# Kernel tuning notes

Hardware: AMD Instinct MI355X
Metric: run time of the kernel (lower is better)

The kernel has to match this reference:

```python
import jax, jax.numpy as jnp
import numpy as np

B, F, V, E = 65536, 39, 100000, 16
EPS = 1e-5

def setup_inputs() -> dict:
    key = jax.random.key(0)
    ks = jax.random.split(key, 10)
    return {
        'Xi': jax.random.randint(ks[0], (B, F, 1), 0, V, dtype=jnp.int64) if jax.config.read('jax_enable_x64') else jax.random.randint(ks[0], (B, F, 1), 0, V, dtype=jnp.int32),
        'Xv': jax.random.uniform(ks[1], (B, F), dtype=jnp.float32),
        'emb1': jax.random.normal(ks[2], (F, V, 1), dtype=jnp.float32),
        'emb2': jax.random.normal(ks[3], (F, V, E), dtype=jnp.float32),
        'W1': jax.random.normal(ks[4], (F * E, 512), dtype=jnp.float32) * 0.02,
        'b1': jax.random.normal(ks[5], (512,), dtype=jnp.float32) * 0.02,
        'g1': jnp.ones((512,), jnp.float32),
        'be1': jnp.zeros((512,), jnp.float32),
        'W2': jax.random.normal(ks[6], (512, 256), dtype=jnp.float32) * 0.02,
        'b2': jax.random.normal(ks[7], (256,), dtype=jnp.float32) * 0.02,
        'g2': jnp.ones((256,), jnp.float32),
        'be2': jnp.zeros((256,), jnp.float32),
        'bias': jax.random.normal(ks[8], (1,), dtype=jnp.float32),
    }

def _batchnorm(x, g, b):
    mu = jnp.mean(x, axis=0)
    var = jnp.mean(jnp.square(x - mu), axis=0)  # biased var, torch BN training mode
    return (x - mu) * jax.lax.rsqrt(var + EPS) * g + b

def reference(Xi, Xv, emb1, emb2, W1, b1, g1, be1, W2, b2, g2, be2, bias):
    idx = Xi[:, :, 0]                                # [B, F]
    fidx = jnp.arange(F)[None, :]                    # [1, F]
    # fused per-field gathers: [B, F] and [B, F, E]
    first = emb1[fidx, idx, 0] * Xv                  # first-order, [B, F]
    fm2 = emb2[fidx, idx] * Xv[:, :, None]           # second-order embeds, [B, F, E]
    sum_emb = jnp.sum(fm2, axis=1)                   # [B, E]
    second = 0.5 * (jnp.square(sum_emb) - jnp.sum(jnp.square(fm2), axis=1))  # [B, E]
    # deep part (note: original forward never applies the final num_classes layer)
    deep = fm2.reshape(B, F * E)
    deep = _batchnorm(deep @ W1 + b1, g1, be1)
    deep = _batchnorm(deep @ W2 + b2, g2, be2)
    return bias + jnp.sum(first, axis=1) + jnp.sum(second, axis=1) + jnp.sum(deep, axis=1)
```

## Files before the change

kernel.cpp:

```cpp
#include <hip/hip_runtime.h>

#define B_ROWS 65536
#define F_FEAT 39
#define V_VOC  100000
#define D_PAD  640
#define BN_EPS 1e-5f

typedef __bf16 bf16x8 __attribute__((ext_vector_type(8)));
typedef float  f32x16 __attribute__((ext_vector_type(16)));

__device__ __forceinline__ unsigned short toBF(float x) {
  unsigned int u = __float_as_uint(x);
  u += 0x7fffu + ((u >> 16) & 1u);
  return (unsigned short)(u >> 16);
}
__device__ __forceinline__ unsigned int pk2(float a, float b) {
  return (unsigned int)toBF(a) | ((unsigned int)toBF(b) << 16);
}

__global__ __launch_bounds__(256) void k0_prep(
    const int* __restrict__ Xi, const float* __restrict__ Xv,
    int* __restrict__ XiT, float* __restrict__ XvT,
    float* __restrict__ M, unsigned short* __restrict__ XT) {
  for (int i = threadIdx.x; i < 800; i += 256)
    M[(size_t)blockIdx.x * 800 + i] = 0.f;

  const int b0 = blockIdx.x * 128;
  for (int u = threadIdx.x; u < 16 * 128; u += 256) {
    int m = 624 + (u >> 7), j = u & 127;
    XT[(size_t)m * B_ROWS + b0 + j] = (m == 624) ? (unsigned short)0x3f80 : (unsigned short)0;
  }

  __shared__ int   ti[128][41];
  __shared__ float tv[128][41];
  for (int u = threadIdx.x; u < 128 * 39; u += 256) {
    int r = u / 39, f = u - r * 39;
    ti[r][f] = Xi[(size_t)b0 * 39 + u];
    tv[r][f] = Xv[(size_t)b0 * 39 + u];
  }
  __syncthreads();
  for (int u = threadIdx.x; u < 39 * 128; u += 256) {
    int f = u >> 7, j = u & 127;
    XiT[(size_t)f * B_ROWS + b0 + j] = ti[j][f];
    XvT[(size_t)f * B_ROWS + b0 + j] = tv[j][f];
  }
}

__global__ __launch_bounds__(1024) void k1g_gather(
    const int* __restrict__ XiT, const float* __restrict__ XvT,
    const float* __restrict__ emb1, const float* __restrict__ emb2,
    unsigned short* __restrict__ XB, float* __restrict__ FS1) {
  const int tid = blockIdx.x * 1024 + threadIdx.x;
  for (int e = tid; e < F_FEAT * B_ROWS; e += 256 * 1024) {
    const int f = e >> 16;
    const int id = XiT[e];
    const float xv = XvT[e];
    const float4* er = reinterpret_cast<const float4*>(emb2 + ((size_t)f * V_VOC + id) * 16);
    float4 q0 = er[0], q1 = er[1], q2 = er[2], q3 = er[3];
    float e1 = emb1[(size_t)f * V_VOC + id];
    uint4 d0, d1;
    d0.x = pk2(q0.x * xv, q0.y * xv); d0.y = pk2(q0.z * xv, q0.w * xv);
    d0.z = pk2(q1.x * xv, q1.y * xv); d0.w = pk2(q1.z * xv, q1.w * xv);
    d1.x = pk2(q2.x * xv, q2.y * xv); d1.y = pk2(q2.z * xv, q2.w * xv);
    d1.z = pk2(q3.x * xv, q3.y * xv); d1.w = pk2(q3.z * xv, q3.w * xv);
    uint4* dst = reinterpret_cast<uint4*>(XB + (size_t)e * 16);
    dst[0] = d0; dst[1] = d1;
    FS1[e] = e1 * xv;
  }
}

__global__ __launch_bounds__(256) void k_transpose(const unsigned short* __restrict__ XB,
                                                   unsigned short* __restrict__ XT) {
  const int f = blockIdx.y;
  const int b0 = blockIdx.x * 512;
  __shared__ unsigned int ls[16][257];
  const int t = threadIdx.x;
  const int bb = b0 + 2 * t;
  const uint4* s0 = reinterpret_cast<const uint4*>(XB + ((size_t)f * B_ROWS + bb) * 16);
  uint4 qa0 = s0[0], qa1 = s0[1], qb0 = s0[2], qb1 = s0[3];
  const unsigned short* pa0 = reinterpret_cast<const unsigned short*>(&qa0);
  const unsigned short* pa1 = reinterpret_cast<const unsigned short*>(&qa1);
  const unsigned short* pb0 = reinterpret_cast<const unsigned short*>(&qb0);
  const unsigned short* pb1 = reinterpret_cast<const unsigned short*>(&qb1);
#pragma unroll
  for (int d = 0; d < 8; ++d) {
    ls[d][t]     = (unsigned)pa0[d] | ((unsigned)pb0[d] << 16);
    ls[d + 8][t] = (unsigned)pa1[d] | ((unsigned)pb1[d] << 16);
  }
  __syncthreads();
#pragma unroll
  for (int d = 0; d < 16; ++d) {
    unsigned int* row = reinterpret_cast<unsigned int*>(
        XT + (size_t)(f * 16 + d) * B_ROWS + b0);
    row[t] = ls[d][t];
  }
}

#define KSPLIT 32
__global__ __launch_bounds__(256) void k2_syrk(const unsigned short* __restrict__ XT,
                                               float* __restrict__ M) {
  const int p = blockIdx.x;
  const int xcd = p & 7;
  const int ks = ((p >> 3) / 15) * 8 + xcd;
  int pair = (p >> 3) % 15;
  int ti = 0;
  while (pair >= 5 - ti) { pair -= 5 - ti; ++ti; }
  const int tj = ti + pair;

  __shared__ unsigned short pa[128 * 64];
  __shared__ unsigned short pb[128 * 64];

  const int lane = threadIdx.x & 63, wid = threadIdx.x >> 6;
  const int wm = wid >> 1, wn = wid & 1;
  const int rl = lane & 31, hh = lane >> 5;

  f32x16 acc00, acc01, acc10, acc11;
#pragma unroll
  for (int i = 0; i < 16; ++i) { acc00[i] = 0.f; acc01[i] = 0.f; acc10[i] = 0.f; acc11[i] = 0.f; }

  const int krange = B_ROWS / KSPLIT;
  const int kbase = ks * krange;

  for (int kt = 0; kt < krange; kt += 64) {
    const int k0 = kbase + kt;
#pragma unroll
    for (int g2 = 0; g2 < 4; ++g2) {
      const int g = threadIdx.x + g2 * 256;
      const int r = g >> 3, j = g & 7;
      uint4 va = *reinterpret_cast<const uint4*>(XT + (size_t)(ti * 128 + r) * B_ROWS + k0 + j * 8);
      *reinterpret_cast<uint4*>((char*)pa + r * 128 + ((j ^ (r & 7)) << 4)) = va;
      uint4 vb = *reinterpret_cast<const uint4*>(XT + (size_t)(tj * 128 + r) * B_ROWS + k0 + j * 8);
      *reinterpret_cast<uint4*>((char*)pb + r * 128 + ((j ^ (r & 7)) << 4)) = vb;
    }
    __syncthreads();
#pragma unroll
    for (int kc = 0; kc < 4; ++kc) {
      const int ra0 = wm * 64 + rl, ra1 = wm * 64 + 32 + rl;
      const int rb0 = wn * 64 + rl, rb1 = wn * 64 + 32 + rl;
      bf16x8 a0 = *reinterpret_cast<const bf16x8*>((char*)pa + ra0 * 128 + (((kc * 2 + hh) ^ (ra0 & 7)) << 4));
      bf16x8 a1 = *reinterpret_cast<const bf16x8*>((char*)pa + ra1 * 128 + (((kc * 2 + hh) ^ (ra1 & 7)) << 4));
      bf16x8 b0 = *reinterpret_cast<const bf16x8*>((char*)pb + rb0 * 128 + (((kc * 2 + hh) ^ (rb0 & 7)) << 4));
      bf16x8 b1 = *reinterpret_cast<const bf16x8*>((char*)pb + rb1 * 128 + (((kc * 2 + hh) ^ (rb1 & 7)) << 4));
      acc00 = __builtin_amdgcn_mfma_f32_32x32x16_bf16(a0, b0, acc00, 0, 0, 0);
      acc01 = __builtin_amdgcn_mfma_f32_32x32x16_bf16(a0, b1, acc01, 0, 0, 0);
      acc10 = __builtin_amdgcn_mfma_f32_32x32x16_bf16(a1, b0, acc10, 0, 0, 0);
      acc11 = __builtin_amdgcn_mfma_f32_32x32x16_bf16(a1, b1, acc11, 0, 0, 0);
    }
    __syncthreads();
  }

#pragma unroll
  for (int rr = 0; rr < 16; ++rr) {
    const int rloc = (rr & 3) + ((rr >> 2) << 3) + hh * 4;
    const int row0 = ti * 128 + wm * 64 + rloc;
    const int row1 = row0 + 32;
    const int col0 = tj * 128 + wn * 64 + rl;
    atomicAdd(&M[row0 * D_PAD + col0], acc00[rr]);
    atomicAdd(&M[row0 * D_PAD + col0 + 32], acc01[rr]);
    atomicAdd(&M[row1 * D_PAD + col0], acc10[rr]);
    atomicAdd(&M[row1 * D_PAD + col0 + 32], acc11[rr]);
  }
}

__device__ __forceinline__ float fetchM(const float* M, int a, int b) {
  if ((a >> 7) > (b >> 7)) { int t = a; a = b; b = t; }
  return M[a * D_PAD + b];
}
__global__ void k3a_cov(const float* __restrict__ M, float* __restrict__ Cov,
                        float* __restrict__ mu) {
  const int i = blockIdx.x;
  const float inv = 1.f / 65536.f;
  const float mui = fetchM(M, 624, i) * inv;
  for (int j = threadIdx.x; j < D_PAD; j += 256) {
    float muj = fetchM(M, 624, j) * inv;
    Cov[i * D_PAD + j] = fetchM(M, i, j) * inv - mui * muj;
    if (i == 0) mu[j] = muj;
  }
}

__global__ __launch_bounds__(256) void qform(const float* __restrict__ Cov,
                                             const float* __restrict__ W, const int ldw,
                                             const float* __restrict__ g,
                                             float* __restrict__ alpha) {
  const int k0 = blockIdx.x * 2;
  __shared__ float w0s[624], w1s[624];
  for (int i = threadIdx.x; i < 624; i += 256) {
    w0s[i] = W[(size_t)i * ldw + k0];
    w1s[i] = W[(size_t)i * ldw + k0 + 1];
  }
  __syncthreads();
  const int j0 = threadIdx.x, j1 = threadIdx.x + 256, j2 = threadIdx.x + 512;
  const bool v2 = (j2 < 624);
  const float wj00 = w0s[j0], wj01 = w0s[j1], wj02 = v2 ? w0s[j2] : 0.f;
  const float wj10 = w1s[j0], wj11 = w1s[j1], wj12 = v2 ? w1s[j2] : 0.f;
  float acc0 = 0.f, acc1 = 0.f;
  for (int i = 0; i < 624; ++i) {
    const float wi0 = w0s[i], wi1 = w1s[i];
    const float* row = Cov + i * D_PAD;
    const float c0 = row[j0], c1 = row[j1], c2 = v2 ? row[j2] : 0.f;
    acc0 += wi0 * (c0 * wj00 + c1 * wj01 + c2 * wj02);
    acc1 += wi1 * (c0 * wj10 + c1 * wj11 + c2 * wj12);
  }
#pragma unroll
  for (int off = 32; off > 0; off >>= 1) {
    acc0 += __shfl_down(acc0, off);
    acc1 += __shfl_down(acc1, off);
  }
  __shared__ float pr[2][4];
  const int lane = threadIdx.x & 63, wv = threadIdx.x >> 6;
  if (lane == 0) { pr[0][wv] = acc0; pr[1][wv] = acc1; }
  __syncthreads();
  if (threadIdx.x == 0) {
    float v0 = pr[0][0] + pr[0][1] + pr[0][2] + pr[0][3];
    float v1 = pr[1][0] + pr[1][1] + pr[1][2] + pr[1][3];
    alpha[k0]     = g[k0]     * rsqrtf(v0 + BN_EPS);
    alpha[k0 + 1] = g[k0 + 1] * rsqrtf(v1 + BN_EPS);
  }
}

__global__ __launch_bounds__(256) void k3c_G(const float* __restrict__ W1,
                                             const float* __restrict__ alpha1,
                                             const float* __restrict__ W2,
                                             float* __restrict__ G) {
  const int i = blockIdx.x;
  __shared__ float a[512];
  for (int k = threadIdx.x; k < 512; k += 256)
    a[k] = W1[(size_t)i * 512 + k] * alpha1[k];
  __syncthreads();
  const int j = threadIdx.x;
  float acc = 0.f;
#pragma unroll 8
  for (int k = 0; k < 512; ++k) acc += a[k] * W2[(size_t)k * 256 + j];
  G[(size_t)i * 256 + j] = acc;
}

__global__ __launch_bounds__(256) void k3e_final(const float* __restrict__ G,
                                                 const float* __restrict__ alpha2,
                                                 const float* __restrict__ mu,
                                                 const float* __restrict__ be2,
                                                 const float* __restrict__ bias,
                                                 float* __restrict__ gw,
                                                 float* __restrict__ consts) {
  __shared__ float a2[256];
  __shared__ float gws[640];
  a2[threadIdx.x] = alpha2[threadIdx.x];
  __syncthreads();
  for (int i = threadIdx.x; i < 640; i += 256) {
    float acc = 0.f;
    if (i < 624) {
      const float* gr = G + (size_t)i * 256;
#pragma unroll 8
      for (int j = 0; j < 256; ++j) acc += gr[j] * a2[j];
    }
    gw[i] = acc;
    gws[i] = acc;
  }
  __syncthreads();
  float pm = 0.f;
  for (int i = threadIdx.x; i < 624; i += 256) pm += mu[i] * gws[i];
  float val = be2[threadIdx.x] - pm;
#pragma unroll
  for (int off = 32; off > 0; off >>= 1) val += __shfl_down(val, off);
  __shared__ float pr[4];
  const int lane = threadIdx.x & 63, wv = threadIdx.x >> 6;
  if (lane == 0) pr[wv] = val;
  __syncthreads();
  if (threadIdx.x == 0) consts[0] = bias[0] + pr[0] + pr[1] + pr[2] + pr[3];
}

__global__ __launch_bounds__(256) void k5_out(const float* __restrict__ FS1,
                                              const unsigned short* __restrict__ XT,
                                              const float* __restrict__ gw,
                                              const float* __restrict__ consts,
                                              float* __restrict__ out) {
  __shared__ float g[624];
  for (int m = threadIdx.x; m < 624; m += 256) g[m] = gw[m];
  __syncthreads();
  const int r = threadIdx.x >> 1, h = threadIdx.x & 1;
  const int b = blockIdx.x * 128 + r;
  const unsigned short* col = XT + b;

  float lin = 0.f, ssq = 0.f;
  float ps[16];
#pragma unroll
  for (int e = 0; e < 16; ++e) ps[e] = 0.f;

  const int m0 = h ? 320 : 0, m1 = h ? 624 : 320;
  for (int mo = m0; mo < m1; mo += 16) {
#pragma unroll
    for (int e = 0; e < 16; ++e) {
      const int m = mo + e;
      float x = __uint_as_float((unsigned int)col[(size_t)m * B_ROWS] << 16);
      lin += g[m] * x;
      ssq += x * x;
      ps[e] += x;
    }
  }
  const int fb = h ? 20 : 0, fe = h ? 39 : 20;
  for (int f = fb; f < fe; ++f)
    lin += FS1[(size_t)f * B_ROWS + b];

  float s2 = 0.f;
#pragma unroll
  for (int e = 0; e < 16; ++e) {
    float t = ps[e] + __shfl_xor(ps[e], 1);
    s2 += t * t;
  }
  float tot = lin + 0.5f * (0.5f * s2 - ssq);
  tot += __shfl_xor(tot, 1);
  if (h == 0) out[b] = tot + consts[0];
}

extern "C" void kernel_launch(void* const* d_in, const int* in_sizes, int n_in,
                              void* d_out, int out_size, void* d_ws, size_t ws_size,
                              hipStream_t stream) {
  const int*   Xi   = (const int*)d_in[0];
  const float* Xv   = (const float*)d_in[1];
  const float* emb1 = (const float*)d_in[2];
  const float* emb2 = (const float*)d_in[3];
  const float* W1   = (const float*)d_in[4];
  const float* g1   = (const float*)d_in[6];
  const float* W2   = (const float*)d_in[8];
  const float* g2   = (const float*)d_in[10];
  const float* be2  = (const float*)d_in[11];
  const float* bias = (const float*)d_in[12];
  float* out = (float*)d_out;
  char* ws = (char*)d_ws;

  const size_t SZ_XT  = (size_t)D_PAD * B_ROWS * 2;
  const size_t SZ_XB  = (size_t)F_FEAT * B_ROWS * 32;
  const size_t SZ_FB  = (size_t)F_FEAT * B_ROWS * 4;

  size_t off = 0;
  unsigned short* XT = (unsigned short*)(ws + off); off += SZ_XT;
  unsigned short* XB = (unsigned short*)(ws + off); off += SZ_XB;
  float* M    = (float*)(ws + off); off += (size_t)D_PAD * D_PAD * 4;
  float* COV  = (float*)(ws + off); off += (size_t)D_PAD * D_PAD * 4;
  float* MU   = (float*)(ws + off); off += D_PAD * 4;
  float* A1   = (float*)(ws + off); off += 512 * 4;
  float* A2   = (float*)(ws + off); off += 256 * 4;
  float* G    = (float*)(ws + off); off += (size_t)624 * 256 * 4;
  float* GW   = (float*)(ws + off); off += D_PAD * 4;
  float* CN   = (float*)(ws + off); off += 256;
  int*   XIT  = (int*)(ws + off);   off += SZ_FB;
  float* XVT  = (float*)(ws + off); off += SZ_FB;
  float* FS1  = (float*)(ws + off); off += SZ_FB;

  k0_prep<<<512, 256, 0, stream>>>(Xi, Xv, XIT, XVT, M, XT);
  k1g_gather<<<256, 1024, 0, stream>>>(XIT, XVT, emb1, emb2, XB, FS1);
  k_transpose<<<dim3(128, F_FEAT), 256, 0, stream>>>(XB, XT);
  k2_syrk<<<15 * KSPLIT, 256, 0, stream>>>(XT, M);
  k3a_cov<<<D_PAD, 256, 0, stream>>>(M, COV, MU);
  qform<<<256, 256, 0, stream>>>(COV, W1, 512, g1, A1);
  k3c_G<<<624, 256, 0, stream>>>(W1, A1, W2, G);
  qform<<<128, 256, 0, stream>>>(COV, G, 256, g2, A2);
  k3e_final<<<1, 256, 0, stream>>>(G, A2, MU, be2, bias, GW, CN);
  k5_out<<<512, 256, 0, stream>>>(FS1, XT, GW, CN, out);
}
```

Measured before the change: 412.7 us.

## Partition embedding gather by XCD with table-half prefetch into L2

The gather is restructured so that each group of blocks sharing an XCD (blockIdx mod 8) handles a fixed set of 78 table slices (field, half-vocab). For each slice the 32 blocks first stream the whole ~3.2MB half-table into the local L2 with coalesced loads, then gather only the rows whose index falls in that half. Output stores are made nontemporal. The aim is to turn random HBM gathers into L2-resident hits. In exchange every index is read twice, the full tables are streamed regardless of use, and the scheme relies on round-robin block-to-XCD placement, with no sync ensuring the prefetch lands before the gathers.

```diff
diff --git a/kernel.cpp b/kernel.cpp
--- a/kernel.cpp
+++ b/kernel.cpp
@@ -3,11 +3,13 @@
 #define B_ROWS 65536
 #define F_FEAT 39
 #define V_VOC  100000
+#define HALF_V 50000
 #define D_PAD  640
 #define BN_EPS 1e-5f
 
 typedef __bf16 bf16x8 __attribute__((ext_vector_type(8)));
 typedef float  f32x16 __attribute__((ext_vector_type(16)));
+typedef unsigned int u32x4 __attribute__((ext_vector_type(4)));
 
 __device__ __forceinline__ unsigned short toBF(float x) {
   unsigned int u = __float_as_uint(x);
@@ -46,26 +48,60 @@
   }
 }
 
-__global__ __launch_bounds__(1024) void k1g_gather(
+__global__ __launch_bounds__(1024) void k1s_gather(
     const int* __restrict__ XiT, const float* __restrict__ XvT,
     const float* __restrict__ emb1, const float* __restrict__ emb2,
     unsigned short* __restrict__ XB, float* __restrict__ FS1) {
-  const int tid = blockIdx.x * 1024 + threadIdx.x;
-  for (int e = tid; e < F_FEAT * B_ROWS; e += 256 * 1024) {
-    const int f = e >> 16;
-    const int id = XiT[e];
-    const float xv = XvT[e];
-    const float4* er = reinterpret_cast<const float4*>(emb2 + ((size_t)f * V_VOC + id) * 16);
-    float4 q0 = er[0], q1 = er[1], q2 = er[2], q3 = er[3];
-    float e1 = emb1[(size_t)f * V_VOC + id];
-    uint4 d0, d1;
-    d0.x = pk2(q0.x * xv, q0.y * xv); d0.y = pk2(q0.z * xv, q0.w * xv);
-    d0.z = pk2(q1.x * xv, q1.y * xv); d0.w = pk2(q1.z * xv, q1.w * xv);
-    d1.x = pk2(q2.x * xv, q2.y * xv); d1.y = pk2(q2.z * xv, q2.w * xv);
-    d1.z = pk2(q3.x * xv, q3.y * xv); d1.w = pk2(q3.z * xv, q3.w * xv);
-    uint4* dst = reinterpret_cast<uint4*>(XB + (size_t)e * 16);
-    dst[0] = d0; dst[1] = d1;
-    FS1[e] = e1 * xv;
+  const int xcd = blockIdx.x & 7;
+  const int sub = blockIdx.x >> 3;
+  const int tid = threadIdx.x;
+  const int sBeg = (xcd < 6) ? xcd * 10 : 60 + (xcd - 6) * 9;
+  const int sEnd = sBeg + ((xcd < 6) ? 10 : 9);
+
+  for (int s = sBeg; s < sEnd; ++s) {
+    const int f = s >> 1;
+    const unsigned vlo = (unsigned)(s & 1) * HALF_V;
+
+    const float4* p2 = reinterpret_cast<const float4*>(emb2 + ((size_t)f * V_VOC + vlo) * 16);
+    const float4* p1 = reinterpret_cast<const float4*>(emb1 + (size_t)f * V_VOC + vlo);
+    float sink = 0.f;
+    const int tpos = sub * 1024 + tid;
+#pragma unroll
+    for (int i = 0; i < 7; ++i) {
+      const int o = tpos + i * 32768;
+      if (o < HALF_V * 4) {
+        float4 q = p2[o];
+        sink += q.x + q.y + q.z + q.w;
+      }
+    }
+    if (tpos < HALF_V / 4) {
+      float4 q = p1[tpos];
+      sink += q.x + q.y + q.z + q.w;
+    }
+    asm volatile("" :: "v"(sink));
+
+    const float* ef  = emb2 + (size_t)f * V_VOC * 16;
+    const float* e1f = emb1 + (size_t)f * V_VOC;
+    const size_t fb = (size_t)f * B_ROWS;
+#pragma unroll
+    for (int it = 0; it < 2; ++it) {
+      const int b = sub * 2048 + it * 1024 + tid;
+      const unsigned id = (unsigned)XiT[fb + b];
+      if (id - vlo < (unsigned)HALF_V) {
+        const float xv = XvT[fb + b];
+        const float4* er = reinterpret_cast<const float4*>(ef + (size_t)id * 16);
+        float4 q0 = er[0], q1 = er[1], q2 = er[2], q3 = er[3];
+        u32x4 d0, d1;
+        d0.x = pk2(q0.x * xv, q0.y * xv); d0.y = pk2(q0.z * xv, q0.w * xv);
+        d0.z = pk2(q1.x * xv, q1.y * xv); d0.w = pk2(q1.z * xv, q1.w * xv);
+        d1.x = pk2(q2.x * xv, q2.y * xv); d1.y = pk2(q2.z * xv, q2.w * xv);
+        d1.z = pk2(q3.x * xv, q3.y * xv); d1.w = pk2(q3.z * xv, q3.w * xv);
+        u32x4* dp = reinterpret_cast<u32x4*>(XB + (fb + b) * 16);
+        __builtin_nontemporal_store(d0, dp);
+        __builtin_nontemporal_store(d1, dp + 1);
+        FS1[fb + b] = e1f[id] * xv;
+      }
+    }
   }
 }
 
@@ -347,7 +383,7 @@
   float* FS1  = (float*)(ws + off); off += SZ_FB;
 
   k0_prep<<<512, 256, 0, stream>>>(Xi, Xv, XIT, XVT, M, XT);
-  k1g_gather<<<256, 1024, 0, stream>>>(XIT, XVT, emb1, emb2, XB, FS1);
+  k1s_gather<<<256, 1024, 0, stream>>>(XIT, XVT, emb1, emb2, XB, FS1);
   k_transpose<<<dim3(128, F_FEAT), 256, 0, stream>>>(XB, XT);
   k2_syrk<<<15 * KSPLIT, 256, 0, stream>>>(XT, M);
   k3a_cov<<<D_PAD, 256, 0, stream>>>(M, COV, MU);
```

Result: no change. 416.5 us (+0.9%).
